# Optimization experiments

Measured on AMD Instinct MI355X. Metric: run time of the kernel, lower is better.

Reference implementation:

```python
import jax, jax.numpy as jnp
import numpy as np

N = 100000   # nodes
E = 1600000  # edges (avg degree 16)
G = 512      # graphs in batch
IN = 96      # in_channels
H = 128      # hidden_channels
C = 100      # num_classes
ED = 8       # edge_dim
L = 4        # num_layers
EPS_LN = 1e-5


def setup_inputs() -> dict:
    key = jax.random.key(0)
    ks = jax.random.split(key, 24)
    s = 0.05
    d = {
        "x": jax.random.normal(ks[0], (N, IN), jnp.float32),
        "edge_index": jax.random.randint(ks[1], (2, E), 0, N, jnp.int32),
        "batch": jnp.sort(jax.random.randint(ks[2], (N,), 0, G, jnp.int32)),
        "edge_attr": jax.random.normal(ks[3], (E, ED), jnp.float32),
        # edge encoder MLP: Linear(ED,H) -> ReLU -> Linear(H,1)
        "ee_W1": jax.random.normal(ks[4], (ED, H), jnp.float32) * s,
        "ee_b1": jnp.zeros((H,), jnp.float32),
        "ee_W2": jax.random.normal(ks[5], (H, 1), jnp.float32) * s,
        "ee_b2": jnp.zeros((1,), jnp.float32),
        # GCNConv weights (PyG: lin without bias, bias added after aggregation)
        "W0": jax.random.normal(ks[6], (IN, H), jnp.float32) * s,
        "cb0": jnp.zeros((H,), jnp.float32),
        "W1": jax.random.normal(ks[7], (H, H), jnp.float32) * s,
        "cb1": jnp.zeros((H,), jnp.float32),
        "W2": jax.random.normal(ks[8], (H, H), jnp.float32) * s,
        "cb2": jnp.zeros((H,), jnp.float32),
        "W3": jax.random.normal(ks[9], (H, H), jnp.float32) * s,
        "cb3": jnp.zeros((H,), jnp.float32),
        # LayerNorm params
        "g0": jnp.ones((H,), jnp.float32), "be0": jnp.zeros((H,), jnp.float32),
        "g1": jnp.ones((H,), jnp.float32), "be1": jnp.zeros((H,), jnp.float32),
        "g2": jnp.ones((H,), jnp.float32), "be2": jnp.zeros((H,), jnp.float32),
        "g3": jnp.ones((H,), jnp.float32), "be3": jnp.zeros((H,), jnp.float32),
        # residual projection for layer 0 only (IN != H)
        "res_W": jax.random.normal(ks[10], (IN, H), jnp.float32) * s,
        "res_b": jnp.zeros((H,), jnp.float32),
        # head: Linear(2H,H) -> ReLU -> Linear(H,C)
        "hW1": jax.random.normal(ks[11], (2 * H, H), jnp.float32) * s,
        "hb1": jnp.zeros((H,), jnp.float32),
        "hW2": jax.random.normal(ks[12], (H, C), jnp.float32) * s,
        "hb2": jnp.zeros((C,), jnp.float32),
    }
    return d


def _layer_norm(h, g, b):
    mu = jnp.mean(h, axis=-1, keepdims=True)
    var = jnp.mean(jnp.square(h - mu), axis=-1, keepdims=True)
    return g * (h - mu) / jnp.sqrt(var + EPS_LN) + b


def reference(x, edge_index, batch, edge_attr,
              ee_W1, ee_b1, ee_W2, ee_b2,
              W0, cb0, W1, cb1, W2, cb2, W3, cb3,
              g0, be0, g1, be1, g2, be2, g3, be3,
              res_W, res_b, hW1, hb1, hW2, hb2):
    row, col = edge_index[0], edge_index[1]

    # edge weight = softplus(MLP(edge_attr)) + 1e-4  -> [E]
    eh = jax.nn.relu(edge_attr @ ee_W1 + ee_b1)
    ew = jax.nn.softplus((eh @ ee_W2 + ee_b2)[:, 0]) + 1e-4

    # add self loops with weight 1 (PyG GCNConv default)
    loops = jnp.arange(N, dtype=row.dtype)
    row_sl = jnp.concatenate([row, loops])
    col_sl = jnp.concatenate([col, loops])
    ew_sl = jnp.concatenate([ew, jnp.ones((N,), ew.dtype)])

    # symmetric normalization: D^-1/2 A D^-1/2 (deg over target index)
    deg = jax.ops.segment_sum(ew_sl, col_sl, num_segments=N)
    dis = jnp.where(deg > 0, jax.lax.rsqrt(deg), 0.0)
    norm = dis[row_sl] * ew_sl * dis[col_sl]  # [E+N]

    def conv(h, W, b):
        hw = h @ W                                   # [N,H]
        msg = hw[row_sl] * norm[:, None]             # [E+N,H]
        return jax.ops.segment_sum(msg, col_sl, num_segments=N) + b

    Ws = [W0, W1, W2, W3]
    cbs = [cb0, cb1, cb2, cb3]
    gs = [g0, g1, g2, g3]
    bes = [be0, be1, be2, be3]

    hidden = []
    cur = x
    for i in range(L):
        h = conv(cur, Ws[i], cbs[i])
        h = _layer_norm(h, gs[i], bes[i])
        res = cur @ res_W + res_b if i == 0 else cur
        h = jax.nn.relu(h + res)
        # dropout: eval mode -> identity
        hidden.append(h)
        cur = h
    xm = jnp.mean(jnp.stack(hidden, axis=0), axis=0)  # [N,H]

    # meanmax pooling over graphs
    counts = jax.ops.segment_sum(jnp.ones((N,), xm.dtype), batch, num_segments=G)
    gmean = jax.ops.segment_sum(xm, batch, num_segments=G) / jnp.maximum(counts, 1.0)[:, None]
    gmax = jax.ops.segment_max(xm, batch, num_segments=G)
    gmax = jnp.where(jnp.isfinite(gmax), gmax, 0.0)
    g = jnp.concatenate([gmean, gmax], axis=-1)       # [G,2H]

    # head (dropout identity in eval)
    return jax.nn.relu(g @ hW1 + hb1) @ hW2 + hb2     # [G,C]
```

## Files before the change

### kernel.cpp

```cpp
#include <hip/hip_runtime.h>
#include <hip/hip_fp16.h>
#include <math.h>

#define NN 100000
#define EE 1600000
#define GB 512
#define INC 96
#define HH 128
#define CC 100
#define MAXD 64
#define BUCKB 9
#define NBUK 196
#define CAPB 10240
#define EB 4096

typedef __bf16 bf16x8 __attribute__((ext_vector_type(8)));
typedef _Float16 f16x8 __attribute__((ext_vector_type(8)));
typedef float f32x4 __attribute__((ext_vector_type(4)));

__device__ __forceinline__ float unpack_w_f32(unsigned v) {
    return __half2float(__ushort_as_half((unsigned short)(v & 0x7FFFu)));
}
__device__ __forceinline__ __half2 unpack_w_h2(unsigned v) {
    __half h = __ushort_as_half((unsigned short)(v & 0x7FFFu));
    return __halves2half2(h, h);
}

__global__ __launch_bounds__(256) void k_cast(const float* __restrict__ src, __half* __restrict__ dst, int n4) {
    int i = blockIdx.x * 256 + threadIdx.x;
    if (i >= n4) return;
    float4 v = *(const float4*)&src[(size_t)i * 4];
    __half2 a = __floats2half2_rn(v.x, v.y);
    __half2 b = __floats2half2_rn(v.z, v.w);
    *(__half2*)&dst[(size_t)i * 4]     = a;
    *(__half2*)&dst[(size_t)i * 4 + 2] = b;
}

__global__ __launch_bounds__(512) void k_prep(
    const float* __restrict__ W0, const float* __restrict__ resW,
    const float* __restrict__ W1m, const float* __restrict__ W2m, const float* __restrict__ W3m,
    const float* __restrict__ eeW1,
    __half* __restrict__ wt0, __half* __restrict__ wtR,
    __half* __restrict__ wt1, __half* __restrict__ wt2, __half* __restrict__ wt3,
    __bf16* __restrict__ w1f)
{
    int tid = threadIdx.x;
    if (blockIdx.x == 288) {
        int t = tid >> 6, lane = tid & 63;
        int ln15 = lane & 15, quad = lane >> 4;
        bf16x8 v = {};
        if (quad == 0) {
#pragma unroll
            for (int j = 0; j < 8; ++j) v[j] = (__bf16)eeW1[j * 128 + t * 16 + ln15];
        }
        *(bf16x8*)&w1f[(size_t)(t * 64 + lane) * 8] = v;
        return;
    }
    if (tid >= 256) return;
    int idx = blockIdx.x * 256 + tid;
    const float* src; __half* dst; int K, base;
    if (idx < 12288)      { src = W0;   dst = wt0; K = 96;  base = 0; }
    else if (idx < 24576) { src = resW; dst = wtR; K = 96;  base = 12288; }
    else if (idx < 40960) { src = W1m;  dst = wt1; K = 128; base = 24576; }
    else if (idx < 57344) { src = W2m;  dst = wt2; K = 128; base = 40960; }
    else if (idx < 73728) { src = W3m;  dst = wt3; K = 128; base = 57344; }
    else return;
    int l = idx - base;
    int k = l >> 7, n = l & 127;
    dst[(size_t)n * K + k] = __float2half(src[l]);
}

__global__ __launch_bounds__(256) void k_edge_mlp_mfma(
    const float* __restrict__ ea,
    const __bf16* __restrict__ w1f, const float* __restrict__ b1,
    const float* __restrict__ W2, const float* __restrict__ b2,
    __half* __restrict__ ew)
{
    __shared__ float sDot[128];
    int tid = threadIdx.x, wva = tid >> 6, lane = tid & 63;
    int ln15 = lane & 15, quad = lane >> 4;
    int ebase = blockIdx.x * 128 + wva * 32;

    bf16x8 bfr[8];
#pragma unroll
    for (int t = 0; t < 8; ++t) bfr[t] = *(const bf16x8*)&w1f[(size_t)(t * 64 + lane) * 8];

    bf16x8 a0 = {}, a1 = {};
    if (quad == 0) {
        const float* p0 = &ea[(size_t)(ebase + ln15) * 8];
        float4 u0 = *(const float4*)p0, u1 = *(const float4*)(p0 + 4);
        a0[0] = (__bf16)u0.x; a0[1] = (__bf16)u0.y; a0[2] = (__bf16)u0.z; a0[3] = (__bf16)u0.w;
        a0[4] = (__bf16)u1.x; a0[5] = (__bf16)u1.y; a0[6] = (__bf16)u1.z; a0[7] = (__bf16)u1.w;
        const float* p1 = &ea[(size_t)(ebase + 16 + ln15) * 8];
        float4 w0 = *(const float4*)p1, w1v = *(const float4*)(p1 + 4);
        a1[0] = (__bf16)w0.x; a1[1] = (__bf16)w0.y; a1[2] = (__bf16)w0.z; a1[3] = (__bf16)w0.w;
        a1[4] = (__bf16)w1v.x; a1[5] = (__bf16)w1v.y; a1[6] = (__bf16)w1v.z; a1[7] = (__bf16)w1v.w;
    }

    f32x4 d0 = {0.f, 0.f, 0.f, 0.f}, d1 = {0.f, 0.f, 0.f, 0.f};
#pragma unroll
    for (int t = 0; t < 8; ++t) {
        f32x4 z = {0.f, 0.f, 0.f, 0.f};
        f32x4 c0 = __builtin_amdgcn_mfma_f32_16x16x32_bf16(a0, bfr[t], z, 0, 0, 0);
        f32x4 c1 = __builtin_amdgcn_mfma_f32_16x16x32_bf16(a1, bfr[t], z, 0, 0, 0);
        int col = t * 16 + ln15;
        float b1v = b1[col], w2v = W2[col];
#pragma unroll
        for (int r = 0; r < 4; ++r) {
            float v0 = fmaxf(c0[r] + b1v, 0.0f);
            float v1 = fmaxf(c1[r] + b1v, 0.0f);
            d0[r] = fmaf(v0, w2v, d0[r]);
            d1[r] = fmaf(v1, w2v, d1[r]);
        }
    }
#pragma unroll
    for (int o = 1; o < 16; o <<= 1) {
#pragma unroll
        for (int r = 0; r < 4; ++r) {
            d0[r] += __shfl_xor(d0[r], o, 64);
            d1[r] += __shfl_xor(d1[r], o, 64);
        }
    }
    if (ln15 == 0) {
#pragma unroll
        for (int r = 0; r < 4; ++r) {
            sDot[wva * 32 + quad * 4 + r]      = d0[r];
            sDot[wva * 32 + 16 + quad * 4 + r] = d1[r];
        }
    }
    __syncthreads();
    if (tid < 128) {
        int e = blockIdx.x * 128 + tid;
        float x = sDot[tid] + b2[0];
        float sp = (x > 20.0f) ? x : log1pf(expf(x));
        ew[e] = __float2half(sp + 1e-4f);
    }
}

__global__ __launch_bounds__(256) void k_split(const int* __restrict__ ei, const __half* __restrict__ ew,
                                               int* __restrict__ cntB, uint2* __restrict__ barr) {
    __shared__ unsigned hist[NBUK];
    __shared__ unsigned gbase[NBUK];
    __shared__ unsigned short rloc[EB];
    int tid = threadIdx.x;
    for (int b = tid; b < NBUK; b += 256) hist[b] = 0;
    __syncthreads();
    int e0 = blockIdx.x * EB;
#pragma unroll
    for (int j = 0; j < EB / 256; ++j) {
        int e = e0 + j * 256 + tid;
        if (e < EE) {
            int c = ei[EE + e];
            rloc[j * 256 + tid] = (unsigned short)atomicAdd(&hist[c >> BUCKB], 1u);
        }
    }
    __syncthreads();
    for (int b = tid; b < NBUK; b += 256)
        gbase[b] = (hist[b] > 0) ? (unsigned)atomicAdd(&cntB[b], (int)hist[b]) : 0u;
    __syncthreads();
#pragma unroll
    for (int j = 0; j < EB / 256; ++j) {
        int e = e0 + j * 256 + tid;
        if (e < EE) {
            int c = ei[EE + e];
            int b = c >> BUCKB;
            unsigned pos = gbase[b] + rloc[j * 256 + tid];
            if (pos < CAPB) {
                unsigned hb = (unsigned)__half_as_ushort(ew[e]) & 0x7FFFu;
                barr[(size_t)b * CAPB + pos] = make_uint2(((unsigned)c << 15) | hb, (unsigned)ei[e]);
            }
        }
    }
}

__global__ __launch_bounds__(256) void k_build(const int* __restrict__ cntB, const uint2* __restrict__ barr,
                                               unsigned* __restrict__ epack, int* __restrict__ cnt,
                                               float* __restrict__ dis) {
    __shared__ unsigned ncnt[512];
    __shared__ float ndeg[512];
    int tid = threadIdx.x, b = blockIdx.x;
    for (int i = tid; i < 512; i += 256) { ncnt[i] = 0; ndeg[i] = 0.0f; }
    __syncthreads();
    int n0 = b << BUCKB;
    int m = cntB[b]; if (m > CAPB) m = CAPB;
    for (int i = tid; i < m; i += 256) {
        uint2 rec = barr[(size_t)b * CAPB + i];
        int c = (int)(rec.x >> 15);
        int cl = c - n0;
        unsigned rank = atomicAdd(&ncnt[cl], 1u);
        if (rank < MAXD) epack[(size_t)c * MAXD + rank] = (rec.y << 15) | (rec.x & 0x7FFFu);
        atomicAdd(&ndeg[cl], unpack_w_f32(rec.x));
    }
    __syncthreads();
    int nn = NN - n0; if (nn > 512) nn = 512;
    for (int i = tid; i < nn; i += 256) {
        unsigned cc = ncnt[i]; if (cc > MAXD) cc = MAXD;
        cnt[n0 + i] = (int)cc;
        dis[n0 + i] = rsqrtf(1.0f + ndeg[i]);
    }
}

__global__ __launch_bounds__(256) void k_norm(const int* __restrict__ cnt, const float* __restrict__ dis,
                                              unsigned* __restrict__ epack, int n) {
    int wv = threadIdx.x >> 6, lane = threadIdx.x & 63;
    int i = blockIdx.x * 4 + wv;
    if (i >= n) return;
    float dc = dis[i];
    if (lane < cnt[i]) {
        unsigned v = epack[(size_t)i * MAXD + lane];
        float wn = dis[v >> 15] * unpack_w_f32(v) * dc;
        unsigned hb = (unsigned)__half_as_ushort(__float2half(wn)) & 0x7FFFu;
        epack[(size_t)i * MAXD + lane] = (v & 0xFFFF8000u) | hb;
    }
}

__global__ __launch_bounds__(256) void k_gemm_f16(
    const __half* __restrict__ A, const __half* __restrict__ Bt,
    const float* __restrict__ bias, __half* __restrict__ C, int M, int K)
{
    int tid = threadIdx.x;
    int wv = tid >> 6, lane = tid & 63;
    int ln15 = lane & 15, quad = lane >> 4;
    int m0 = blockIdx.x * 64;
    int n0 = wv * 32;
    f32x4 acc[4][2];
#pragma unroll
    for (int mt = 0; mt < 4; ++mt)
#pragma unroll
        for (int nt = 0; nt < 2; ++nt) acc[mt][nt] = (f32x4){0.f, 0.f, 0.f, 0.f};

    int rowm[4];
#pragma unroll
    for (int mt = 0; mt < 4; ++mt) {
        int r = m0 + mt * 16 + ln15;
        rowm[mt] = r < M ? r : M - 1;
    }
    for (int kc = 0; kc < K; kc += 32) {
        f16x8 af[4], bfr[2];
#pragma unroll
        for (int mt = 0; mt < 4; ++mt)
            af[mt] = *(const f16x8*)&A[(size_t)rowm[mt] * K + kc + quad * 8];
#pragma unroll
        for (int nt = 0; nt < 2; ++nt)
            bfr[nt] = *(const f16x8*)&Bt[(size_t)(n0 + nt * 16 + ln15) * K + kc + quad * 8];
#pragma unroll
        for (int mt = 0; mt < 4; ++mt)
#pragma unroll
            for (int nt = 0; nt < 2; ++nt)
                acc[mt][nt] = __builtin_amdgcn_mfma_f32_16x16x32_f16(af[mt], bfr[nt], acc[mt][nt], 0, 0, 0);
    }
#pragma unroll
    for (int nt = 0; nt < 2; ++nt) {
        int col = n0 + nt * 16 + ln15;
        float bv = bias ? bias[col] : 0.0f;
#pragma unroll
        for (int mt = 0; mt < 4; ++mt) {
#pragma unroll
            for (int r = 0; r < 4; ++r) {
                int row = m0 + mt * 16 + quad * 4 + r;
                if (row < M) C[(size_t)row * 128 + col] = __float2half(acc[mt][nt][r] + bv);
            }
        }
    }
}

__global__ __launch_bounds__(256) void k_gemm_dual(
    const __half* __restrict__ A, const __half* __restrict__ Bt1, const __half* __restrict__ Bt2,
    const float* __restrict__ bias2, __half* __restrict__ C1, __half* __restrict__ C2, int M, int K)
{
    int tid = threadIdx.x;
    int wv = tid >> 6, lane = tid & 63;
    int ln15 = lane & 15, quad = lane >> 4;
    int m0 = blockIdx.x * 64;
    int n0 = wv * 32;
    f32x4 acc1[4][2], acc2[4][2];
#pragma unroll
    for (int mt = 0; mt < 4; ++mt)
#pragma unroll
        for (int nt = 0; nt < 2; ++nt) {
            acc1[mt][nt] = (f32x4){0.f, 0.f, 0.f, 0.f};
            acc2[mt][nt] = (f32x4){0.f, 0.f, 0.f, 0.f};
        }
    int rowm[4];
#pragma unroll
    for (int mt = 0; mt < 4; ++mt) {
        int r = m0 + mt * 16 + ln15;
        rowm[mt] = r < M ? r : M - 1;
    }
    for (int kc = 0; kc < K; kc += 32) {
        f16x8 af[4], bf1[2], bf2[2];
#pragma unroll
        for (int mt = 0; mt < 4; ++mt)
            af[mt] = *(const f16x8*)&A[(size_t)rowm[mt] * K + kc + quad * 8];
#pragma unroll
        for (int nt = 0; nt < 2; ++nt) {
            bf1[nt] = *(const f16x8*)&Bt1[(size_t)(n0 + nt * 16 + ln15) * K + kc + quad * 8];
            bf2[nt] = *(const f16x8*)&Bt2[(size_t)(n0 + nt * 16 + ln15) * K + kc + quad * 8];
        }
#pragma unroll
        for (int mt = 0; mt < 4; ++mt)
#pragma unroll
            for (int nt = 0; nt < 2; ++nt) {
                acc1[mt][nt] = __builtin_amdgcn_mfma_f32_16x16x32_f16(af[mt], bf1[nt], acc1[mt][nt], 0, 0, 0);
                acc2[mt][nt] = __builtin_amdgcn_mfma_f32_16x16x32_f16(af[mt], bf2[nt], acc2[mt][nt], 0, 0, 0);
            }
    }
#pragma unroll
    for (int nt = 0; nt < 2; ++nt) {
        int col = n0 + nt * 16 + ln15;
        float bv2 = bias2[col];
#pragma unroll
        for (int mt = 0; mt < 4; ++mt) {
#pragma unroll
            for (int r = 0; r < 4; ++r) {
                int row = m0 + mt * 16 + quad * 4 + r;
                if (row < M) {
                    C1[(size_t)row * 128 + col] = __float2half(acc1[mt][nt][r]);
                    C2[(size_t)row * 128 + col] = __float2half(acc2[mt][nt][r] + bv2);
                }
            }
        }
    }
}

__global__ __launch_bounds__(256) void k_agg_ln(
    const __half* __restrict__ hw, const float* __restrict__ dis,
    const int* __restrict__ cnt, const unsigned* __restrict__ epack,
    const float* __restrict__ cb, const float* __restrict__ gam,
    const float* __restrict__ bet, const __half* __restrict__ res,
    __half* __restrict__ out, int n)
{
    int wv = threadIdx.x >> 6;
    int lane = threadIdx.x & 63;
    int i = blockIdx.x * 4 + wv;
    if (i >= n) return;
    float di = dis[i];
    float sn = di * di;
    __half2 own = *(const __half2*)&hw[(size_t)i * HH + lane * 2];
    __half hsn = __float2half(sn);
    __half2 acca = __hmul2(own, __halves2half2(hsn, hsn));
    __half2 accb = __halves2half2(__float2half(0.0f), __float2half(0.0f));
    int cn = cnt[i];
    const unsigned* ebase = &epack[(size_t)i * MAXD];
    int k = 0;
    for (; k + 8 <= cn; k += 8) {
        uint4 q0 = *(const uint4*)&ebase[k];
        uint4 q1 = *(const uint4*)&ebase[k + 4];
        __half2 v0 = *(const __half2*)&hw[(size_t)(q0.x >> 15) * HH + lane * 2];
        __half2 v1 = *(const __half2*)&hw[(size_t)(q0.y >> 15) * HH + lane * 2];
        __half2 v2 = *(const __half2*)&hw[(size_t)(q0.z >> 15) * HH + lane * 2];
        __half2 v3 = *(const __half2*)&hw[(size_t)(q0.w >> 15) * HH + lane * 2];
        __half2 v4 = *(const __half2*)&hw[(size_t)(q1.x >> 15) * HH + lane * 2];
        __half2 v5 = *(const __half2*)&hw[(size_t)(q1.y >> 15) * HH + lane * 2];
        __half2 v6 = *(const __half2*)&hw[(size_t)(q1.z >> 15) * HH + lane * 2];
        __half2 v7 = *(const __half2*)&hw[(size_t)(q1.w >> 15) * HH + lane * 2];
        acca = __hfma2(v0, unpack_w_h2(q0.x), acca);
        accb = __hfma2(v4, unpack_w_h2(q1.x), accb);
        acca = __hfma2(v1, unpack_w_h2(q0.y), acca);
        accb = __hfma2(v5, unpack_w_h2(q1.y), accb);
        acca = __hfma2(v2, unpack_w_h2(q0.z), acca);
        accb = __hfma2(v6, unpack_w_h2(q1.z), accb);
        acca = __hfma2(v3, unpack_w_h2(q0.w), acca);
        accb = __hfma2(v7, unpack_w_h2(q1.w), accb);
    }
    for (; k < cn; ++k) {
        unsigned e = ebase[k];
        __half2 v = *(const __half2*)&hw[(size_t)(e >> 15) * HH + lane * 2];
        acca = __hfma2(v, unpack_w_h2(e), acca);
    }
    __half2 acc = __hadd2(acca, accb);
    float2 af = __half22float2(acc);
    float2 cbv = *(const float2*)&cb[lane * 2];
    af.x += cbv.x; af.y += cbv.y;
    float s1 = af.x + af.y;
    float s2 = af.x * af.x + af.y * af.y;
#pragma unroll
    for (int o = 32; o > 0; o >>= 1) {
        s1 += __shfl_xor(s1, o, 64);
        s2 += __shfl_xor(s2, o, 64);
    }
    float mean = s1 * (1.0f / HH);
    float var = fmaxf(s2 * (1.0f / HH) - mean * mean, 0.0f);
    float rstd = rsqrtf(var + 1e-5f);
    float2 gv = *(const float2*)&gam[lane * 2];
    float2 bv = *(const float2*)&bet[lane * 2];
    float2 rv = __half22float2(*(const __half2*)&res[(size_t)i * HH + lane * 2]);
    float hx = fmaxf(fmaf(gv.x, (af.x - mean) * rstd, bv.x) + rv.x, 0.0f);
    float hy = fmaxf(fmaf(gv.y, (af.y - mean) * rstd, bv.y) + rv.y, 0.0f);
    *(__half2*)&out[(size_t)i * HH + lane * 2] = __floats2half2_rn(hx, hy);
}

__global__ __launch_bounds__(512) void k_pool_head(
    const __half* __restrict__ l0, const __half* __restrict__ l1,
    const __half* __restrict__ l2, const __half* __restrict__ l3,
    const int* __restrict__ batch,
    const float* __restrict__ hW1, const float* __restrict__ hb1,
    const float* __restrict__ hW2, const float* __restrict__ hb2,
    float* __restrict__ out, int n)
{
    __shared__ float ssum[8][128];
    __shared__ float smax[8][128];
    __shared__ __align__(16) float sg[256];
    __shared__ __align__(16) float sh[128];
    int g = blockIdx.x, tid = threadIdx.x;
    int grp = tid >> 6, lane = tid & 63;
    int lo = 0, hi = n;
    while (lo < hi) { int m = (lo + hi) >> 1; if (batch[m] < g) lo = m + 1; else hi = m; }
    int start = lo;
    lo = start; hi = n;
    while (lo < hi) { int m = (lo + hi) >> 1; if (batch[m] < g + 1) lo = m + 1; else hi = m; }
    int end = lo;
    float sx = 0.0f, sy = 0.0f, mx = -INFINITY, my = -INFINITY;
    for (int nd = start + grp; nd < end; nd += 8) {
        size_t off = (size_t)nd * HH + lane * 2;
        float2 v0 = __half22float2(*(const __half2*)&l0[off]);
        float2 v1 = __half22float2(*(const __half2*)&l1[off]);
        float2 v2 = __half22float2(*(const __half2*)&l2[off]);
        float2 v3 = __half22float2(*(const __half2*)&l3[off]);
        float vx = (v0.x + v1.x + v2.x + v3.x) * 0.25f;
        float vy = (v0.y + v1.y + v2.y + v3.y) * 0.25f;
        sx += vx; sy += vy;
        mx = fmaxf(mx, vx); my = fmaxf(my, vy);
    }
    ssum[grp][lane * 2] = sx; ssum[grp][lane * 2 + 1] = sy;
    smax[grp][lane * 2] = mx; smax[grp][lane * 2 + 1] = my;
    __syncthreads();
    if (tid < 128) {
        float s = 0.0f, m = -INFINITY;
#pragma unroll
        for (int j = 0; j < 8; ++j) {
            s += ssum[j][tid];
            m = fmaxf(m, smax[j][tid]);
        }
        int cntg = end - start;
        sg[tid] = s / fmaxf((float)cntg, 1.0f);
        sg[128 + tid] = (cntg > 0) ? m : 0.0f;
    }
    __syncthreads();
    if (tid < 128) {
        float h = hb1[tid];
        for (int k = 0; k < 256; ++k) h = fmaf(sg[k], hW1[(size_t)k * 128 + tid], h);
        sh[tid] = fmaxf(h, 0.0f);
    }
    __syncthreads();
    if (tid < 100) {
        float o = hb2[tid];
        for (int k = 0; k < 128; ++k) o = fmaf(sh[k], hW2[(size_t)k * 100 + tid], o);
        out[(size_t)g * 100 + tid] = o;
    }
}

extern "C" void kernel_launch(void* const* d_in, const int* in_sizes, int n_in,
                              void* d_out, int out_size, void* d_ws, size_t ws_size,
                              hipStream_t stream) {
    const float* x     = (const float*)d_in[0];
    const int*   ei    = (const int*)d_in[1];
    const int*   batch = (const int*)d_in[2];
    const float* ea    = (const float*)d_in[3];
    const float* eeW1  = (const float*)d_in[4];
    const float* eeb1  = (const float*)d_in[5];
    const float* eeW2  = (const float*)d_in[6];
    const float* eeb2  = (const float*)d_in[7];
    const float* W[4]  = {(const float*)d_in[8], (const float*)d_in[10], (const float*)d_in[12], (const float*)d_in[14]};
    const float* cb[4] = {(const float*)d_in[9], (const float*)d_in[11], (const float*)d_in[13], (const float*)d_in[15]};
    const float* gm[4] = {(const float*)d_in[16], (const float*)d_in[18], (const float*)d_in[20], (const float*)d_in[22]};
    const float* be[4] = {(const float*)d_in[17], (const float*)d_in[19], (const float*)d_in[21], (const float*)d_in[23]};
    const float* resW  = (const float*)d_in[24];
    const float* resb  = (const float*)d_in[25];
    const float* hW1   = (const float*)d_in[26];
    const float* hb1   = (const float*)d_in[27];
    const float* hW2   = (const float*)d_in[28];
    const float* hb2   = (const float*)d_in[29];
    float* out = (float*)d_out;

    char* w = (char*)d_ws;
    auto alloc = [&](size_t bytes) { void* p = w; w += (bytes + 255) & ~(size_t)255; return p; };
    __half*   ew     = (__half*)  alloc((size_t)EE * 2);
    float*    dis    = (float*)   alloc((size_t)NN * 4);
    int*      cnt    = (int*)     alloc((size_t)NN * 4);
    int*      cntB   = (int*)     alloc((size_t)NBUK * 4);
    uint2*    barr   = (uint2*)   alloc((size_t)NBUK * CAPB * 8);
    unsigned* epack  = (unsigned*)alloc((size_t)(NN * MAXD + 64) * 4);
    __half*   xb     = (__half*)  alloc((size_t)NN * INC * 2);
    __half*   hw     = (__half*)  alloc((size_t)NN * HH * 2);
    __half*   lout[4];
    for (int i = 0; i < 4; ++i) lout[i] = (__half*)alloc((size_t)NN * HH * 2);
    __half*   wt0    = (__half*)  alloc((size_t)INC * HH * 2);
    __half*   wtR    = (__half*)  alloc((size_t)INC * HH * 2);
    __half*   wt1    = (__half*)  alloc((size_t)HH * HH * 2);
    __half*   wt2    = (__half*)  alloc((size_t)HH * HH * 2);
    __half*   wt3    = (__half*)  alloc((size_t)HH * HH * 2);
    __bf16*   w1f    = (__bf16*)  alloc((size_t)8 * 64 * 8 * 2);
    __half*   wtc[4] = {wt0, wt1, wt2, wt3};
    __half*   res0   = lout[1];

    int nblkEdge = EE / 128;
    int nblkSplit = (EE + EB - 1) / EB;
    int nblkGemm = (NN + 63) / 64;
    int nblkCast = (NN * INC / 4 + 255) / 256;

    hipMemsetAsync(cntB, 0, (size_t)NBUK * 4, stream);
    k_cast<<<nblkCast, 256, 0, stream>>>(x, xb, NN * INC / 4);
    k_prep<<<289, 512, 0, stream>>>(W[0], resW, W[1], W[2], W[3], eeW1,
                                    wt0, wtR, wt1, wt2, wt3, w1f);
    k_edge_mlp_mfma<<<nblkEdge, 256, 0, stream>>>(ea, w1f, eeb1, eeW2, eeb2, ew);
    k_split<<<nblkSplit, 256, 0, stream>>>(ei, ew, cntB, barr);
    k_build<<<NBUK, 256, 0, stream>>>(cntB, barr, epack, cnt, dis);
    k_norm<<<(NN + 3) / 4, 256, 0, stream>>>(cnt, dis, epack, NN);

    k_gemm_dual<<<nblkGemm, 256, 0, stream>>>(xb, wt0, wtR, resb, hw, res0, NN, INC);
    k_agg_ln<<<(NN + 3) / 4, 256, 0, stream>>>(hw, dis, cnt, epack,
                                               cb[0], gm[0], be[0], res0, lout[0], NN);
    for (int l = 1; l < 4; ++l) {
        k_gemm_f16<<<nblkGemm, 256, 0, stream>>>(lout[l - 1], wtc[l], nullptr, hw, NN, HH);
        k_agg_ln<<<(NN + 3) / 4, 256, 0, stream>>>(hw, dis, cnt, epack,
                                                   cb[l], gm[l], be[l], lout[l - 1], lout[l], NN);
    }

    k_pool_head<<<GB, 512, 0, stream>>>(lout[0], lout[1], lout[2], lout[3], batch,
                                        hW1, hb1, hW2, hb2, out, NN);
}
```

Before: 754.2 us.

## Fold symmetric GCN normalization into GEMM epilogue and drop cast/norm kernels

```diff
diff --git a/kernel.cpp b/kernel.cpp
--- a/kernel.cpp
+++ b/kernel.cpp
@@ -24,16 +24,6 @@
 __device__ __forceinline__ __half2 unpack_w_h2(unsigned v) {
     __half h = __ushort_as_half((unsigned short)(v & 0x7FFFu));
     return __halves2half2(h, h);
-}
-
-__global__ __launch_bounds__(256) void k_cast(const float* __restrict__ src, __half* __restrict__ dst, int n4) {
-    int i = blockIdx.x * 256 + threadIdx.x;
-    if (i >= n4) return;
-    float4 v = *(const float4*)&src[(size_t)i * 4];
-    __half2 a = __floats2half2_rn(v.x, v.y);
-    __half2 b = __floats2half2_rn(v.z, v.w);
-    *(__half2*)&dst[(size_t)i * 4]     = a;
-    *(__half2*)&dst[(size_t)i * 4 + 2] = b;
 }
 
 __global__ __launch_bounds__(512) void k_prep(
@@ -200,23 +190,9 @@
     }
 }
 
-__global__ __launch_bounds__(256) void k_norm(const int* __restrict__ cnt, const float* __restrict__ dis,
-                                              unsigned* __restrict__ epack, int n) {
-    int wv = threadIdx.x >> 6, lane = threadIdx.x & 63;
-    int i = blockIdx.x * 4 + wv;
-    if (i >= n) return;
-    float dc = dis[i];
-    if (lane < cnt[i]) {
-        unsigned v = epack[(size_t)i * MAXD + lane];
-        float wn = dis[v >> 15] * unpack_w_f32(v) * dc;
-        unsigned hb = (unsigned)__half_as_ushort(__float2half(wn)) & 0x7FFFu;
-        epack[(size_t)i * MAXD + lane] = (v & 0xFFFF8000u) | hb;
-    }
-}
-
 __global__ __launch_bounds__(256) void k_gemm_f16(
     const __half* __restrict__ A, const __half* __restrict__ Bt,
-    const float* __restrict__ bias, __half* __restrict__ C, int M, int K)
+    const float* __restrict__ dis, __half* __restrict__ C, int M, int K)
 {
     int tid = threadIdx.x;
     int wv = tid >> 6, lane = tid & 63;
@@ -252,21 +228,21 @@
 #pragma unroll
     for (int nt = 0; nt < 2; ++nt) {
         int col = n0 + nt * 16 + ln15;
-        float bv = bias ? bias[col] : 0.0f;
 #pragma unroll
         for (int mt = 0; mt < 4; ++mt) {
 #pragma unroll
             for (int r = 0; r < 4; ++r) {
                 int row = m0 + mt * 16 + quad * 4 + r;
-                if (row < M) C[(size_t)row * 128 + col] = __float2half(acc[mt][nt][r] + bv);
+                if (row < M) C[(size_t)row * 128 + col] = __float2half(acc[mt][nt][r] * dis[row]);
             }
         }
     }
 }
 
 __global__ __launch_bounds__(256) void k_gemm_dual(
-    const __half* __restrict__ A, const __half* __restrict__ Bt1, const __half* __restrict__ Bt2,
-    const float* __restrict__ bias2, __half* __restrict__ C1, __half* __restrict__ C2, int M, int K)
+    const float* __restrict__ A, const __half* __restrict__ Bt1, const __half* __restrict__ Bt2,
+    const float* __restrict__ bias2, const float* __restrict__ dis,
+    __half* __restrict__ C1, __half* __restrict__ C2, int M, int K)
 {
     int tid = threadIdx.x;
     int wv = tid >> 6, lane = tid & 63;
@@ -290,8 +266,14 @@
     for (int kc = 0; kc < K; kc += 32) {
         f16x8 af[4], bf1[2], bf2[2];
 #pragma unroll
-        for (int mt = 0; mt < 4; ++mt)
-            af[mt] = *(const f16x8*)&A[(size_t)rowm[mt] * K + kc + quad * 8];
+        for (int mt = 0; mt < 4; ++mt) {
+            const float* ap = &A[(size_t)rowm[mt] * K + kc + quad * 8];
+            float4 u0 = *(const float4*)ap, u1 = *(const float4*)(ap + 4);
+            af[mt][0] = (_Float16)u0.x; af[mt][1] = (_Float16)u0.y;
+            af[mt][2] = (_Float16)u0.z; af[mt][3] = (_Float16)u0.w;
+            af[mt][4] = (_Float16)u1.x; af[mt][5] = (_Float16)u1.y;
+            af[mt][6] = (_Float16)u1.z; af[mt][7] = (_Float16)u1.w;
+        }
 #pragma unroll
         for (int nt = 0; nt < 2; ++nt) {
             bf1[nt] = *(const f16x8*)&Bt1[(size_t)(n0 + nt * 16 + ln15) * K + kc + quad * 8];
@@ -315,7 +297,7 @@
             for (int r = 0; r < 4; ++r) {
                 int row = m0 + mt * 16 + quad * 4 + r;
                 if (row < M) {
-                    C1[(size_t)row * 128 + col] = __float2half(acc1[mt][nt][r]);
+                    C1[(size_t)row * 128 + col] = __float2half(acc1[mt][nt][r] * dis[row]);
                     C2[(size_t)row * 128 + col] = __float2half(acc2[mt][nt][r] + bv2);
                 }
             }
@@ -335,10 +317,7 @@
     int i = blockIdx.x * 4 + wv;
     if (i >= n) return;
     float di = dis[i];
-    float sn = di * di;
-    __half2 own = *(const __half2*)&hw[(size_t)i * HH + lane * 2];
-    __half hsn = __float2half(sn);
-    __half2 acca = __hmul2(own, __halves2half2(hsn, hsn));
+    __half2 acca = *(const __half2*)&hw[(size_t)i * HH + lane * 2];
     __half2 accb = __halves2half2(__float2half(0.0f), __float2half(0.0f));
     int cn = cnt[i];
     const unsigned* ebase = &epack[(size_t)i * MAXD];
@@ -371,7 +350,8 @@
     __half2 acc = __hadd2(acca, accb);
     float2 af = __half22float2(acc);
     float2 cbv = *(const float2*)&cb[lane * 2];
-    af.x += cbv.x; af.y += cbv.y;
+    af.x = fmaf(di, af.x, cbv.x);
+    af.y = fmaf(di, af.y, cbv.y);
     float s1 = af.x + af.y;
     float s2 = af.x * af.x + af.y * af.y;
 #pragma unroll
@@ -481,7 +461,6 @@
     int*      cntB   = (int*)     alloc((size_t)NBUK * 4);
     uint2*    barr   = (uint2*)   alloc((size_t)NBUK * CAPB * 8);
     unsigned* epack  = (unsigned*)alloc((size_t)(NN * MAXD + 64) * 4);
-    __half*   xb     = (__half*)  alloc((size_t)NN * INC * 2);
     __half*   hw     = (__half*)  alloc((size_t)NN * HH * 2);
     __half*   lout[4];
     for (int i = 0; i < 4; ++i) lout[i] = (__half*)alloc((size_t)NN * HH * 2);
@@ -497,22 +476,19 @@
     int nblkEdge = EE / 128;
     int nblkSplit = (EE + EB - 1) / EB;
     int nblkGemm = (NN + 63) / 64;
-    int nblkCast = (NN * INC / 4 + 255) / 256;
 
     hipMemsetAsync(cntB, 0, (size_t)NBUK * 4, stream);
-    k_cast<<<nblkCast, 256, 0, stream>>>(x, xb, NN * INC / 4);
     k_prep<<<289, 512, 0, stream>>>(W[0], resW, W[1], W[2], W[3], eeW1,
                                     wt0, wtR, wt1, wt2, wt3, w1f);
     k_edge_mlp_mfma<<<nblkEdge, 256, 0, stream>>>(ea, w1f, eeb1, eeW2, eeb2, ew);
     k_split<<<nblkSplit, 256, 0, stream>>>(ei, ew, cntB, barr);
     k_build<<<NBUK, 256, 0, stream>>>(cntB, barr, epack, cnt, dis);
-    k_norm<<<(NN + 3) / 4, 256, 0, stream>>>(cnt, dis, epack, NN);
-
-    k_gemm_dual<<<nblkGemm, 256, 0, stream>>>(xb, wt0, wtR, resb, hw, res0, NN, INC);
+
+    k_gemm_dual<<<nblkGemm, 256, 0, stream>>>(x, wt0, wtR, resb, dis, hw, res0, NN, INC);
     k_agg_ln<<<(NN + 3) / 4, 256, 0, stream>>>(hw, dis, cnt, epack,
                                                cb[0], gm[0], be[0], res0, lout[0], NN);
     for (int l = 1; l < 4; ++l) {
-        k_gemm_f16<<<nblkGemm, 256, 0, stream>>>(lout[l - 1], wtc[l], nullptr, hw, NN, HH);
+        k_gemm_f16<<<nblkGemm, 256, 0, stream>>>(lout[l - 1], wtc[l], dis, hw, NN, HH);
         k_agg_ln<<<(NN + 3) / 4, 256, 0, stream>>>(hw, dis, cnt, epack,
                                                    cb[l], gm[l], be[l], lout[l - 1], lout[l], NN);
     }
```

New measurement: 750.2 us. No clear change (-0.5%).
